# Performance work log

Measured on AMD Instinct MI355X. Metric: run time of the kernel, lower is better.

The kernel has to match this reference:

```python
import jax, jax.numpy as jnp
import numpy as np

B, S, H = 1, 2048, 3584
NH, NKV, D = 16, 8, 256
GROUPS = NH // NKV
WINDOW = 1024
SOFTCAP = 50.0
SCALING = 256.0 ** -0.5  # query_pre_attn_scalar ** -0.5
MASK_VAL = -1e9


def rotate_half(x):
    x1, x2 = jnp.split(x, 2, axis=-1)
    return jnp.concatenate([-x2, x1], axis=-1)


def setup_inputs() -> dict:
    key = jax.random.key(0)
    ks = jax.random.split(key, 5)
    hidden_states = jax.random.normal(ks[0], (B, S, H), dtype=jnp.float32)
    # real rotary embeddings, HF convention: [B, S, head_dim]
    inv_freq = 1.0 / (10000.0 ** (np.arange(0, D, 2, dtype=np.float32) / D))
    freqs = np.arange(S, dtype=np.float32)[:, None] * inv_freq[None, :]  # [S, D/2]
    emb = np.concatenate([freqs, freqs], axis=-1)  # [S, D]
    cos = jnp.asarray(np.cos(emb))[None]  # [1, S, D]
    sin = jnp.asarray(np.sin(emb))[None]
    sc = 1.0 / np.sqrt(H)
    wq = jax.random.normal(ks[1], (NH * D, H), dtype=jnp.float32) * sc
    wk = jax.random.normal(ks[2], (NKV * D, H), dtype=jnp.float32) * sc
    wv = jax.random.normal(ks[3], (NKV * D, H), dtype=jnp.float32) * sc
    wo = jax.random.normal(ks[4], (H, NH * D), dtype=jnp.float32) * (1.0 / np.sqrt(NH * D))
    return {"hidden_states": hidden_states, "cos": cos, "sin": sin,
            "wq": wq, "wk": wk, "wv": wv, "wo": wo}


def reference(hidden_states, cos, sin, wq, wk, wv, wo):
    # QKV projections -> [B, n_heads, S, D]
    q = jnp.einsum('bsh,oh->bso', hidden_states, wq).reshape(B, S, NH, D).transpose(0, 2, 1, 3)
    k = jnp.einsum('bsh,oh->bso', hidden_states, wk).reshape(B, S, NKV, D).transpose(0, 2, 1, 3)
    v = jnp.einsum('bsh,oh->bso', hidden_states, wv).reshape(B, S, NKV, D).transpose(0, 2, 1, 3)
    # RoPE (cos/sin broadcast over head dim)
    c = cos[:, None, :, :]
    s = sin[:, None, :, :]
    q = q * c + rotate_half(q) * s
    k = k * c + rotate_half(k) * s
    # GQA: repeat KV heads
    k = jnp.repeat(k, GROUPS, axis=1)  # [B, NH, S, D]
    v = jnp.repeat(v, GROUPS, axis=1)
    # scores + logit soft-capping (tanh), then causal + sliding-window mask
    scores = jnp.einsum('bhqd,bhkd->bhqk', q, k) * SCALING
    scores = SOFTCAP * jnp.tanh(scores / SOFTCAP)
    idx = jnp.arange(S)
    allowed = (idx[None, :] <= idx[:, None]) & (idx[:, None] - idx[None, :] < WINDOW)  # [S, S]
    scores = jnp.where(allowed[None, None], scores, MASK_VAL)
    p = jax.nn.softmax(scores, axis=-1)
    out = jnp.einsum('bhqk,bhkd->bhqd', p, v)  # [B, NH, S, D]
    out = out.transpose(0, 2, 1, 3).reshape(B, S, NH * D)
    return jnp.einsum('bso,ho->bsh', out, wo)
```

## Files before the change

kernel.cpp:

```cpp
#include <hip/hip_runtime.h>
#include <stdint.h>

#define S_LEN 2048
#define HDIM  3584
#define NHEAD 16
#define NKVH  8
#define DHEAD 256
#define QD    (NHEAD * DHEAD)
#define KD    (NKVH * DHEAD)
#define QKVD  (QD + 2 * KD)
#define WINDOW 1024
#define MASK_VAL (-1e9f)

typedef __bf16 bf16x8 __attribute__((ext_vector_type(8)));
typedef float  f32x4  __attribute__((ext_vector_type(4)));

__device__ __forceinline__ float bf2f(ushort u) {
    union { uint32_t i; float f; } v; v.i = ((uint32_t)u) << 16; return v.f;
}
__device__ __forceinline__ ushort f2bf(float f) {
    union { float f; uint32_t i; } v; v.f = f;
    uint32_t r = (v.i + 0x7FFF + ((v.i >> 16) & 1)) >> 16;
    return (ushort)r;
}
__device__ __forceinline__ void gll16(const ushort* g, ushort* l) {
    __builtin_amdgcn_global_load_lds(
        (const __attribute__((address_space(1))) void*)g,
        (__attribute__((address_space(3))) void*)l, 16, 0, 0);
}

#define N_H8  (S_LEN * HDIM / 8)
#define N_WQ8 (QD * HDIM / 8)
#define N_WK8 (KD * HDIM / 8)
#define N_WO8 (HDIM * QD / 8)
#define N_CVT (N_H8 + N_WQ8 + 2 * N_WK8 + N_WO8)

__global__ __launch_bounds__(256) void cvt5_kernel(
    const float* __restrict__ hid, const float* __restrict__ wq,
    const float* __restrict__ wk,  const float* __restrict__ wv,
    const float* __restrict__ wo,
    ushort* __restrict__ hb, ushort* __restrict__ wb, ushort* __restrict__ ob)
{
    int j = blockIdx.x * blockDim.x + threadIdx.x;
    const float* s; ushort* d;
    if (j < N_H8)                { s = hid; d = hb; }
    else if ((j -= N_H8) < N_WQ8)  { s = wq; d = wb; }
    else if ((j -= N_WQ8) < N_WK8) { s = wk; d = wb + (size_t)QD * HDIM; }
    else if ((j -= N_WK8) < N_WK8) { s = wv; d = wb + (size_t)(QD + KD) * HDIM; }
    else                         { j -= N_WK8; s = wo; d = ob; }
    float4 a = ((const float4*)s)[(size_t)j * 2];
    float4 b = ((const float4*)s)[(size_t)j * 2 + 1];
    ushort tmp[8];
    tmp[0] = f2bf(a.x); tmp[1] = f2bf(a.y); tmp[2] = f2bf(a.z); tmp[3] = f2bf(a.w);
    tmp[4] = f2bf(b.x); tmp[5] = f2bf(b.y); tmp[6] = f2bf(b.z); tmp[7] = f2bf(b.w);
    ((uint4*)d)[j] = *(uint4*)tmp;
}

__global__ __launch_bounds__(256) void cvt_kernel(const float* __restrict__ src,
                                                  ushort* __restrict__ dst, int n8)
{
    int i = blockIdx.x * blockDim.x + threadIdx.x;
    if (i >= n8) return;
    float4 a = ((const float4*)src)[i * 2];
    float4 b = ((const float4*)src)[i * 2 + 1];
    ushort tmp[8];
    tmp[0] = f2bf(a.x); tmp[1] = f2bf(a.y); tmp[2] = f2bf(a.z); tmp[3] = f2bf(a.w);
    tmp[4] = f2bf(b.x); tmp[5] = f2bf(b.y); tmp[6] = f2bf(b.z); tmp[7] = f2bf(b.w);
    ((uint4*)dst)[i] = *(uint4*)tmp;
}

__device__ __forceinline__ void stage_f32(ushort* __restrict__ dst,
                                          const float* __restrict__ src,
                                          int r0, int K, int kt, int t)
{
#pragma unroll
    for (int i = 0; i < 4; i++) {
        int g = t + i * 256;
        int row = g >> 3, c = g & 7;
        float4 f = *(const float4*)(src + (size_t)(r0 + row) * K + kt + c * 4);
        ushort4 u;
        u.x = f2bf(f.x); u.y = f2bf(f.y); u.z = f2bf(f.z); u.w = f2bf(f.w);
        int cl = (c >> 1) ^ ((row >> 1) & 3);
        *(ushort4*)(dst + row * 32 + cl * 8 + (c & 1) * 4) = u;
    }
}

template <typename TA, typename TC>
__global__ __launch_bounds__(256) void gemm_async(const TA* __restrict__ A,
                                                  const ushort* __restrict__ B,
                                                  TC* __restrict__ C,
                                                  int M, int N, int K)
{
    __shared__ __align__(16) ushort As[128 * 32];
    __shared__ __align__(16) ushort Bs[128 * 32];

    const int t    = threadIdx.x;
    const int lane = t & 63;
    const int w    = t >> 6;
    const int l15  = lane & 15;
    const int quad = lane >> 4;
    const int m0   = blockIdx.y * 128;
    const int n0   = blockIdx.x * 128;
    const int wm   = (w >> 1) * 64;
    const int wn   = (w & 1) * 64;
    const int srow = lane >> 2;
    const int scol = ((lane & 3) ^ ((srow >> 1) & 3)) * 8;
    const int sw   = (l15 >> 1) & 3;

    f32x4 acc[4][4] = {};

    for (int kt = 0; kt < K; kt += 32) {
        __syncthreads();
#pragma unroll
        for (int j = 0; j < 2; j++) {
            const int rb = w * 32 + j * 16;
            if constexpr (sizeof(TA) == 2) {
                gll16((const ushort*)A + (size_t)(m0 + rb + srow) * K + kt + scol,
                      As + rb * 32);
            }
            gll16(B + (size_t)(n0 + rb + srow) * K + kt + scol, Bs + rb * 32);
        }
        if constexpr (sizeof(TA) == 4)
            stage_f32(As, (const float*)A, m0, K, kt, t);
        __syncthreads();

        bf16x8 a[4], b[4];
#pragma unroll
        for (int mi = 0; mi < 4; mi++)
            a[mi] = *(const bf16x8*)(As + (wm + mi * 16 + l15) * 32 + (quad ^ sw) * 8);
#pragma unroll
        for (int ni = 0; ni < 4; ni++)
            b[ni] = *(const bf16x8*)(Bs + (wn + ni * 16 + l15) * 32 + (quad ^ sw) * 8);
#pragma unroll
        for (int mi = 0; mi < 4; mi++)
#pragma unroll
            for (int ni = 0; ni < 4; ni++)
                acc[mi][ni] = __builtin_amdgcn_mfma_f32_16x16x32_bf16(
                    a[mi], b[ni], acc[mi][ni], 0, 0, 0);
    }

#pragma unroll
    for (int mi = 0; mi < 4; mi++)
#pragma unroll
        for (int ni = 0; ni < 4; ni++)
#pragma unroll
            for (int r = 0; r < 4; r++) {
                int row = m0 + wm + mi * 16 + quad * 4 + r;
                int col = n0 + wn + ni * 16 + l15;
                float val = acc[mi][ni][r];
                if constexpr (sizeof(TC) == 4) C[(size_t)row * N + col] = val;
                else                           C[(size_t)row * N + col] = f2bf(val);
            }
}

__global__ __launch_bounds__(256) void gemm_sync(const float* __restrict__ A,
                                                 const float* __restrict__ B,
                                                 ushort* __restrict__ C,
                                                 int M, int N, int K)
{
    __shared__ __align__(16) ushort As[128 * 32];
    __shared__ __align__(16) ushort Bs[128 * 32];
    const int t = threadIdx.x, lane = t & 63, w = t >> 6;
    const int l15 = lane & 15, quad = lane >> 4;
    const int sw = (l15 >> 1) & 3;
    const int m0 = blockIdx.y * 128, n0 = blockIdx.x * 128;
    const int wm = (w >> 1) * 64, wn = (w & 1) * 64;
    f32x4 acc[4][4] = {};
    for (int kt = 0; kt < K; kt += 32) {
        __syncthreads();
        stage_f32(As, A, m0, K, kt, t);
        stage_f32(Bs, B, n0, K, kt, t);
        __syncthreads();
        bf16x8 a[4], b[4];
#pragma unroll
        for (int mi = 0; mi < 4; mi++)
            a[mi] = *(const bf16x8*)(As + (wm + mi * 16 + l15) * 32 + (quad ^ sw) * 8);
#pragma unroll
        for (int ni = 0; ni < 4; ni++)
            b[ni] = *(const bf16x8*)(Bs + (wn + ni * 16 + l15) * 32 + (quad ^ sw) * 8);
#pragma unroll
        for (int mi = 0; mi < 4; mi++)
#pragma unroll
            for (int ni = 0; ni < 4; ni++)
                acc[mi][ni] = __builtin_amdgcn_mfma_f32_16x16x32_bf16(
                    a[mi], b[ni], acc[mi][ni], 0, 0, 0);
    }
#pragma unroll
    for (int mi = 0; mi < 4; mi++)
#pragma unroll
        for (int ni = 0; ni < 4; ni++)
#pragma unroll
            for (int r = 0; r < 4; r++)
                C[(size_t)(m0 + wm + mi * 16 + quad * 4 + r) * N +
                  n0 + wn + ni * 16 + l15] = f2bf(acc[mi][ni][r]);
}

__global__ __launch_bounds__(256) void gemm_sync_hf(const ushort* __restrict__ A,
                                                    const float* __restrict__ B,
                                                    float* __restrict__ C,
                                                    int M, int N, int K)
{
    __shared__ __align__(16) ushort As[128 * 32];
    __shared__ __align__(16) ushort Bs[128 * 32];
    const int t = threadIdx.x, lane = t & 63, w = t >> 6;
    const int l15 = lane & 15, quad = lane >> 4;
    const int sw = (l15 >> 1) & 3;
    const int m0 = blockIdx.y * 128, n0 = blockIdx.x * 128;
    const int wm = (w >> 1) * 64, wn = (w & 1) * 64;
    f32x4 acc[4][4] = {};
    for (int kt = 0; kt < K; kt += 32) {
        __syncthreads();
#pragma unroll
        for (int i = 0; i < 2; i++) {
            int g = t + i * 256;
            int row = g >> 2, c = g & 3;
            int cl = c ^ ((row >> 1) & 3);
            *(uint4*)(As + row * 32 + cl * 8) =
                *(const uint4*)(A + (size_t)(m0 + row) * K + kt + c * 8);
        }
        stage_f32(Bs, B, n0, K, kt, t);
        __syncthreads();
        bf16x8 a[4], b[4];
#pragma unroll
        for (int mi = 0; mi < 4; mi++)
            a[mi] = *(const bf16x8*)(As + (wm + mi * 16 + l15) * 32 + (quad ^ sw) * 8);
#pragma unroll
        for (int ni = 0; ni < 4; ni++)
            b[ni] = *(const bf16x8*)(Bs + (wn + ni * 16 + l15) * 32 + (quad ^ sw) * 8);
#pragma unroll
        for (int mi = 0; mi < 4; mi++)
#pragma unroll
            for (int ni = 0; ni < 4; ni++)
                acc[mi][ni] = __builtin_amdgcn_mfma_f32_16x16x32_bf16(
                    a[mi], b[ni], acc[mi][ni], 0, 0, 0);
    }
#pragma unroll
    for (int mi = 0; mi < 4; mi++)
#pragma unroll
        for (int ni = 0; ni < 4; ni++)
#pragma unroll
            for (int r = 0; r < 4; r++)
                C[(size_t)(m0 + wm + mi * 16 + quad * 4 + r) * N +
                  n0 + wn + ni * 16 + l15] = acc[mi][ni][r];
}

__global__ void rope_kernel(ushort* __restrict__ x, int stride,
                            const float* __restrict__ cosb,
                            const float* __restrict__ sinb, int nh)
{
    int idx  = blockIdx.x * blockDim.x + threadIdx.x;
    int d    = idx & 127;
    int rest = idx >> 7;
    int h    = rest & (nh - 1);
    int s    = rest / nh;
    size_t base = (size_t)s * stride + h * DHEAD;
    float c  = cosb[s * DHEAD + d];
    float sn = sinb[s * DHEAD + d];
    float x1 = bf2f(x[base + d]);
    float x2 = bf2f(x[base + d + 128]);
    x[base + d]       = f2bf(x1 * c - x2 * sn);
    x[base + d + 128] = f2bf(x2 * c + x1 * sn);
}

__global__ __launch_bounds__(256) void vtrans_kernel(const ushort* __restrict__ v,
                                                     int stride,
                                                     ushort* __restrict__ vt)
{
    __shared__ __align__(16) ushort tile[64][72];
    int s0 = blockIdx.x * 64, c0 = blockIdx.y * 64;
    int t  = threadIdx.x;
#pragma unroll
    for (int i = 0; i < 2; i++) {
        int cI = t + i * 256;
        int row = cI >> 3, c8 = cI & 7;
        *(uint4*)&tile[row][c8 * 8] =
            *(const uint4*)(v + (size_t)(s0 + row) * stride + c0 + c8 * 8);
    }
    __syncthreads();
#pragma unroll
    for (int i = 0; i < 2; i++) {
        int cI = t + i * 256;
        int crow = cI >> 3, s8 = cI & 7;
        ushort tmp[8];
#pragma unroll
        for (int j = 0; j < 8; j++) tmp[j] = tile[s8 * 8 + j][crow];
        *(uint4*)(vt + (size_t)(c0 + crow) * S_LEN + s0 + s8 * 8) = *(uint4*)tmp;
    }
}

template <typename TO>
__global__ __launch_bounds__(256) void attn_kernel(const ushort* __restrict__ qr, int qstride,
                                                   const ushort* __restrict__ kr, int kstride,
                                                   const ushort* __restrict__ vt,
                                                   TO* __restrict__ out)
{
    __shared__ __align__(16) ushort Ks[64 * 256];
    __shared__ __align__(16) ushort Vs[256 * 64];
    __shared__ __align__(16) ushort Ps[4][16 * 68];

    const int t    = threadIdx.x;
    const int lane = t & 63;
    const int w    = t >> 6;
    const int l15  = lane & 15;
    const int quad = lane >> 4;
    const int q0B  = blockIdx.x * 64;
    const int q0   = q0B + w * 16;
    const int h    = blockIdx.y;
    const int kvh  = h >> 1;

    bf16x8 aQ[8];
    const ushort* qrow = qr + (size_t)(q0 + l15) * qstride + h * DHEAD;
#pragma unroll
    for (int kk = 0; kk < 8; kk++)
        aQ[kk] = *(const bf16x8*)(qrow + kk * 32 + quad * 8);

    f32x4 oacc[16] = {};
    float m_i[4], l_i[4];
#pragma unroll
    for (int r = 0; r < 4; r++) { m_i[r] = -1e30f; l_i[r] = 0.f; }

    int km = q0B - (WINDOW - 1);
    if (km < 0) km = 0;
    km &= ~63;

    for (int kb = km; kb < q0B + 64; kb += 64) {
        __syncthreads();
#pragma unroll
        for (int i = 0; i < 8; i++) {
            int base = i * 256 + w * 64;
            int idx  = base + lane;
            int row = idx >> 5, c = idx & 31;
            int cs = c ^ (row & 7);
            gll16(kr + (size_t)(kb + row) * kstride + kvh * DHEAD + cs * 8,
                  Ks + base * 8);
        }
#pragma unroll
        for (int i = 0; i < 8; i++) {
            int base = i * 256 + w * 64;
            int idx  = base + lane;
            int row = idx >> 3, c = idx & 7;
            int cs = c ^ (row & 7);
            gll16(vt + (size_t)(kvh * DHEAD + row) * S_LEN + kb + cs * 8,
                  Vs + base * 8);
        }
        __syncthreads();

        f32x4 sc[4] = {};
#pragma unroll
        for (int ni = 0; ni < 4; ni++) {
            int row = ni * 16 + l15;
#pragma unroll
            for (int kk = 0; kk < 8; kk++) {
                int cp = (kk * 4 + quad) ^ (row & 7);
                bf16x8 bk = *(const bf16x8*)(Ks + row * 256 + cp * 8);
                sc[ni] = __builtin_amdgcn_mfma_f32_16x16x32_bf16(aQ[kk], bk, sc[ni], 0, 0, 0);
            }
        }

        const bool interior = (kb + 63 <= q0) && (q0 + 15 - kb < WINDOW);
        float p[4][4];
        float mt[4] = { -1e30f, -1e30f, -1e30f, -1e30f };
        if (interior) {
#pragma unroll
            for (int ni = 0; ni < 4; ni++)
#pragma unroll
                for (int r = 0; r < 4; r++) {
                    float e = __expf(sc[ni][r] * 0.0025f);
                    float x = 50.f * (e - 1.f) * __builtin_amdgcn_rcpf(e + 1.f);
                    p[ni][r] = x;
                    mt[r] = fmaxf(mt[r], x);
                }
        } else {
#pragma unroll
            for (int ni = 0; ni < 4; ni++)
#pragma unroll
                for (int r = 0; r < 4; r++) {
                    int qi = q0 + quad * 4 + r;
                    int ki = kb + ni * 16 + l15;
                    float e = __expf(sc[ni][r] * 0.0025f);
                    float x = 50.f * (e - 1.f) * __builtin_amdgcn_rcpf(e + 1.f);
                    bool ok = (ki <= qi) && (qi - ki < WINDOW);
                    x = ok ? x : MASK_VAL;
                    p[ni][r] = x;
                    mt[r] = fmaxf(mt[r], x);
                }
        }
#pragma unroll
        for (int r = 0; r < 4; r++)
#pragma unroll
            for (int off = 1; off < 16; off <<= 1)
                mt[r] = fmaxf(mt[r], __shfl_xor(mt[r], off));

        float alpha[4], rs[4];
#pragma unroll
        for (int r = 0; r < 4; r++) {
            float mn = fmaxf(m_i[r], mt[r]);
            alpha[r] = __expf(m_i[r] - mn);
            m_i[r] = mn;
            rs[r] = 0.f;
        }
#pragma unroll
        for (int ni = 0; ni < 4; ni++)
#pragma unroll
            for (int r = 0; r < 4; r++) {
                float pe = __expf(p[ni][r] - m_i[r]);
                rs[r] += pe;
                Ps[w][(quad * 4 + r) * 68 + ni * 16 + l15] = f2bf(pe);
            }
#pragma unroll
        for (int r = 0; r < 4; r++) {
#pragma unroll
            for (int off = 1; off < 16; off <<= 1)
                rs[r] += __shfl_xor(rs[r], off);
            l_i[r] = l_i[r] * alpha[r] + rs[r];
        }
#pragma unroll
        for (int nd = 0; nd < 16; nd++)
#pragma unroll
            for (int r = 0; r < 4; r++)
                oacc[nd][r] *= alpha[r];

        __asm__ volatile("s_waitcnt lgkmcnt(0)" ::: "memory");

        bf16x8 aP[2];
#pragma unroll
        for (int kk = 0; kk < 2; kk++)
            aP[kk] = *(const bf16x8*)(&Ps[w][l15 * 68 + kk * 32 + quad * 8]);
#pragma unroll
        for (int nd = 0; nd < 16; nd++) {
            int row = nd * 16 + l15;
#pragma unroll
            for (int kk = 0; kk < 2; kk++) {
                int cp = (kk * 4 + quad) ^ (row & 7);
                bf16x8 bv = *(const bf16x8*)(Vs + row * 64 + cp * 8);
                oacc[nd] = __builtin_amdgcn_mfma_f32_16x16x32_bf16(aP[kk], bv, oacc[nd], 0, 0, 0);
            }
        }
    }

#pragma unroll
    for (int r = 0; r < 4; r++) {
        float invl = __builtin_amdgcn_rcpf(l_i[r]);
#pragma unroll
        for (int nd = 0; nd < 16; nd++) {
            int qi = q0 + quad * 4 + r;
            int d  = nd * 16 + l15;
            float val = oacc[nd][r] * invl;
            if constexpr (sizeof(TO) == 4) out[(size_t)qi * QD + h * DHEAD + d] = val;
            else                           out[(size_t)qi * QD + h * DHEAD + d] = f2bf(val);
        }
    }
}

extern "C" void kernel_launch(void* const* d_in, const int* in_sizes, int n_in,
                              void* d_out, int out_size, void* d_ws, size_t ws_size,
                              hipStream_t stream)
{
    const float* hidden = (const float*)d_in[0];
    const float* cosb   = (const float*)d_in[1];
    const float* sinb   = (const float*)d_in[2];
    const float* wq     = (const float*)d_in[3];
    const float* wk     = (const float*)d_in[4];
    const float* wv     = (const float*)d_in[5];
    const float* wo     = (const float*)d_in[6];
    float* outp = (float*)d_out;

    const size_t nH   = (size_t)S_LEN * HDIM;
    const size_t nWQ  = (size_t)QD * HDIM;
    const size_t nWK  = (size_t)KD * HDIM;
    const size_t nWB  = (size_t)QKVD * HDIM;
    const size_t nWO  = (size_t)HDIM * QD;
    const size_t nQKV = (size_t)S_LEN * QKVD;
    const size_t nAT  = (size_t)S_LEN * QD;
    const size_t nVT  = (size_t)S_LEN * KD;

    dim3 blk(256);
    const size_t needA = (nWB + nQKV + nH + nWO) * 2;
    const size_t needB = (nWB + nQKV) * 2;

    if (ws_size >= needA) {
        ushort* wb  = (ushort*)d_ws;
        ushort* qkv = wb + nWB;
        ushort* hb  = qkv + nQKV;
        ushort* ob  = hb + nH;
        ushort* at  = wb;
        ushort* vtb = wb + nAT;

        cvt5_kernel<<<(N_CVT + 255) / 256, blk, 0, stream>>>(hidden, wq, wk, wv, wo, hb, wb, ob);
        gemm_async<ushort, ushort><<<dim3(QKVD / 128, S_LEN / 128), blk, 0, stream>>>(
            hb, wb, qkv, S_LEN, QKVD, HDIM);
        rope_kernel<<<(S_LEN * NHEAD * 128) / 256, blk, 0, stream>>>(qkv, QKVD, cosb, sinb, NHEAD);
        rope_kernel<<<(S_LEN * NKVH * 128) / 256, blk, 0, stream>>>(qkv + QD, QKVD, cosb, sinb, NKVH);
        vtrans_kernel<<<dim3(S_LEN / 64, KD / 64), blk, 0, stream>>>(qkv + QD + KD, QKVD, vtb);
        attn_kernel<ushort><<<dim3(S_LEN / 64, NHEAD), blk, 0, stream>>>(
            qkv, QKVD, qkv + QD, QKVD, vtb, at);
        gemm_async<ushort, float><<<dim3(HDIM / 128, S_LEN / 128), blk, 0, stream>>>(
            at, ob, outp, S_LEN, HDIM, QD);
    } else if (ws_size >= needB) {
        ushort* wb  = (ushort*)d_ws;
        ushort* qkv = wb + nWB;
        ushort* at  = wb;
        ushort* vtb = wb + nAT;
        ushort* ob  = wb + nAT + nVT;

        cvt_kernel<<<(int)(nWQ / 8 / 256), blk, 0, stream>>>(wq, wb, (int)(nWQ / 8));
        cvt_kernel<<<(int)(nWK / 8 / 256), blk, 0, stream>>>(wk, wb + nWQ, (int)(nWK / 8));
        cvt_kernel<<<(int)(nWK / 8 / 256), blk, 0, stream>>>(wv, wb + nWQ + nWK, (int)(nWK / 8));
        gemm_async<float, ushort><<<dim3(QKVD / 128, S_LEN / 128), blk, 0, stream>>>(
            hidden, wb, qkv, S_LEN, QKVD, HDIM);
        cvt_kernel<<<(int)(nWO / 8 / 256), blk, 0, stream>>>(wo, ob, (int)(nWO / 8));
        rope_kernel<<<(S_LEN * NHEAD * 128) / 256, blk, 0, stream>>>(qkv, QKVD, cosb, sinb, NHEAD);
        rope_kernel<<<(S_LEN * NKVH * 128) / 256, blk, 0, stream>>>(qkv + QD, QKVD, cosb, sinb, NKVH);
        vtrans_kernel<<<dim3(S_LEN / 64, KD / 64), blk, 0, stream>>>(qkv + QD + KD, QKVD, vtb);
        attn_kernel<ushort><<<dim3(S_LEN / 64, NHEAD), blk, 0, stream>>>(
            qkv, QKVD, qkv + QD, QKVD, vtb, at);
        gemm_async<ushort, float><<<dim3(HDIM / 128, S_LEN / 128), blk, 0, stream>>>(
            at, ob, outp, S_LEN, HDIM, QD);
    } else {
        ushort* q   = (ushort*)d_ws;
        ushort* k   = q + nAT;
        ushort* v   = k + nVT;
        ushort* vtb = v + nVT;
        ushort* at  = vtb + nVT;

        gemm_sync<<<dim3(QD / 128, S_LEN / 128), blk, 0, stream>>>(hidden, wq, q, S_LEN, QD, HDIM);
        gemm_sync<<<dim3(KD / 128, S_LEN / 128), blk, 0, stream>>>(hidden, wk, k, S_LEN, KD, HDIM);
        gemm_sync<<<dim3(KD / 128, S_LEN / 128), blk, 0, stream>>>(hidden, wv, v, S_LEN, KD, HDIM);
        rope_kernel<<<(S_LEN * NHEAD * 128) / 256, blk, 0, stream>>>(q, QD, cosb, sinb, NHEAD);
        rope_kernel<<<(S_LEN * NKVH * 128) / 256, blk, 0, stream>>>(k, KD, cosb, sinb, NKVH);
        vtrans_kernel<<<dim3(S_LEN / 64, KD / 64), blk, 0, stream>>>(v, KD, vtb);
        attn_kernel<ushort><<<dim3(S_LEN / 64, NHEAD), blk, 0, stream>>>(q, QD, k, KD, vtb, at);
        gemm_sync_hf<<<dim3(HDIM / 128, S_LEN / 128), blk, 0, stream>>>(at, wo, outp, S_LEN, HDIM, QD);
    }
}
```

Baseline: 631.1 us.

## Add 256x256-tile eight-wave GEMM with double-buffered ping-pong phases

Adds a new bf16 MFMA GEMM kernel using 256x256 output tiles, 512 threads and 64-wide K tiles. It double-buffers global-to-LDS async loads across eight sub-phases per K step, with explicit vmcnt waits, barriers and s_setprio around the MFMA bursts. The QKV projection and output projection use it in place of the 128x128 kernel. Larger tiles raise data reuse per LDS load and the phase schedule overlaps loads with compute. The cost is fewer blocks (e.g. 14x8 for the output GEMM), which may leave CUs idle, and a fragile hand-written wait schedule.

```diff
diff --git a/kernel.cpp b/kernel.cpp
--- a/kernel.cpp
+++ b/kernel.cpp
@@ -85,6 +85,133 @@
     }
 }
 
+#define VM6   asm volatile("s_waitcnt vmcnt(6)" ::: "memory")
+#define VM0   asm volatile("s_waitcnt vmcnt(0)" ::: "memory")
+#define LGKM0 asm volatile("s_waitcnt lgkmcnt(0)" ::: "memory")
+#define MFEN  asm volatile("" ::: "memory")
+
+#define PHASE(BUF, QM, QN, LA, LB, STAGE, TWAIT) do {                          \
+    if (LA) {                                                                  \
+      _Pragma("unroll") for (int i_ = 0; i_ < 4; i_++) {                       \
+        int R_ = wm + (QM) * 64 + i_ * 16 + l15;                               \
+        afr[i_][0] = *(const bf16x8*)(&As[BUF][R_ * 64 + ((quad ^ (R_ & 7)) * 8)]);       \
+        afr[i_][1] = *(const bf16x8*)(&As[BUF][R_ * 64 + (((4 + quad) ^ (R_ & 7)) * 8)]); \
+      }                                                                        \
+    }                                                                          \
+    if (LB) {                                                                  \
+      _Pragma("unroll") for (int n_ = 0; n_ < 2; n_++) {                       \
+        int R_ = wn + (QN) * 32 + n_ * 16 + l15;                               \
+        bfr[n_][0] = *(const bf16x8*)(&Bs[BUF][R_ * 64 + ((quad ^ (R_ & 7)) * 8)]);       \
+        bfr[n_][1] = *(const bf16x8*)(&Bs[BUF][R_ * 64 + (((4 + quad) ^ (R_ & 7)) * 8)]); \
+      }                                                                        \
+    }                                                                          \
+    STAGE;                                                                     \
+    MFEN;                                                                      \
+    __builtin_amdgcn_s_barrier();                                              \
+    LGKM0;                                                                     \
+    __builtin_amdgcn_s_setprio(1);                                             \
+    _Pragma("unroll") for (int i_ = 0; i_ < 4; i_++)                           \
+      _Pragma("unroll") for (int n_ = 0; n_ < 2; n_++) {                       \
+        acc[(QM) * 4 + i_][(QN) * 2 + n_] = __builtin_amdgcn_mfma_f32_16x16x32_bf16(  \
+            afr[i_][0], bfr[n_][0], acc[(QM) * 4 + i_][(QN) * 2 + n_], 0, 0, 0);      \
+        acc[(QM) * 4 + i_][(QN) * 2 + n_] = __builtin_amdgcn_mfma_f32_16x16x32_bf16(  \
+            afr[i_][1], bfr[n_][1], acc[(QM) * 4 + i_][(QN) * 2 + n_], 0, 0, 0);      \
+      }                                                                        \
+    __builtin_amdgcn_s_setprio(0);                                             \
+    TWAIT;                                                                     \
+    __builtin_amdgcn_s_barrier();                                              \
+    MFEN;                                                                      \
+  } while (0)
+
+template <typename TC>
+__global__ __launch_bounds__(512, 2) void gemm256(const ushort* __restrict__ A,
+                                                  const ushort* __restrict__ B,
+                                                  TC* __restrict__ C,
+                                                  int M, int N, int K)
+{
+    __shared__ __align__(16) ushort As[2][256 * 64];
+    __shared__ __align__(16) ushort Bs[2][256 * 64];
+
+    const int t    = threadIdx.x;
+    const int lane = t & 63;
+    const int w    = t >> 6;
+    const int l15  = lane & 15;
+    const int quad = lane >> 4;
+    const int m0   = blockIdx.y * 256;
+    const int n0   = blockIdx.x * 256;
+    const int wm   = (w >> 2) * 128;
+    const int wn   = (w & 3) * 64;
+    const int lr8  = lane >> 3;
+    const int sc   = lane & 7;
+
+    f32x4 acc[8][4] = {};
+    bf16x8 afr[4][2], bfr[2][2];
+
+    auto stageA = [&](int buf, int qm, int tile) {
+#pragma unroll
+        for (int i = 0; i < 2; i++) {
+            int cb  = (i * 8 + w) * 8;
+            int lr  = cb + lr8;
+            int row = qm * 64 + (lr & 63) + ((lr >> 6) << 7);
+            int rb  = qm * 64 + (cb & 63) + ((cb >> 6) << 7);
+            gll16(A + (size_t)(m0 + row) * K + tile * 64 + ((sc ^ lr8) * 8),
+                  &As[buf][rb * 64]);
+        }
+    };
+    auto stageB = [&](int buf, int qn, int tile) {
+#pragma unroll
+        for (int i = 0; i < 2; i++) {
+            int cb  = (i * 8 + w) * 8;
+            int lr  = cb + lr8;
+            int row = ((lr >> 5) << 6) + qn * 32 + (lr & 31);
+            int rb  = ((cb >> 5) << 6) + qn * 32 + (cb & 31);
+            gll16(B + (size_t)(n0 + row) * K + tile * 64 + ((sc ^ lr8) * 8),
+                  &Bs[buf][rb * 64]);
+        }
+    };
+
+    stageB(0, 0, 0);
+    stageA(0, 1, 0);
+    stageA(0, 0, 0);
+    stageB(0, 1, 0);
+    stageB(1, 0, 1);
+    stageA(1, 1, 1);
+    VM6;
+    __builtin_amdgcn_s_barrier();
+    MFEN;
+
+    const int NJ = K >> 7;
+    for (int j = 0; j < NJ; ++j) {
+        const int T = 2 * j;
+        const bool tl = (j == NJ - 1);
+        PHASE(0, 0, 0, 1, 1, stageA(1, 0, T + 1), MFEN);
+        PHASE(0, 1, 0, 1, 0, stageB(1, 1, T + 1), if (tl) { VM0; } else { VM6; });
+        PHASE(0, 1, 1, 0, 1, if (!tl) { stageB(0, 0, T + 2); }, MFEN);
+        PHASE(0, 0, 1, 1, 0, if (!tl) { stageA(0, 1, T + 2); }, if (!tl) { VM6; } else { MFEN; });
+        PHASE(1, 0, 0, 1, 1, if (!tl) { stageA(0, 0, T + 2); }, MFEN);
+        PHASE(1, 1, 0, 1, 0, if (!tl) { stageB(0, 1, T + 2); }, if (!tl) { VM6; } else { MFEN; });
+        PHASE(1, 1, 1, 0, 1, if (!tl) { stageB(1, 0, T + 3); }, MFEN);
+        PHASE(1, 0, 1, 1, 0, if (!tl) { stageA(1, 1, T + 3); }, if (!tl) { VM6; } else { MFEN; });
+    }
+
+#pragma unroll
+    for (int qm = 0; qm < 2; qm++)
+#pragma unroll
+      for (int i = 0; i < 4; i++)
+#pragma unroll
+        for (int qn = 0; qn < 2; qn++)
+#pragma unroll
+          for (int n = 0; n < 2; n++)
+#pragma unroll
+            for (int r = 0; r < 4; r++) {
+                int row = m0 + wm + qm * 64 + i * 16 + quad * 4 + r;
+                int col = n0 + wn + qn * 32 + n * 16 + l15;
+                float val = acc[qm * 4 + i][qn * 2 + n][r];
+                if constexpr (sizeof(TC) == 4) C[(size_t)row * N + col] = val;
+                else                           C[(size_t)row * N + col] = f2bf(val);
+            }
+}
+
 template <typename TA, typename TC>
 __global__ __launch_bounds__(256) void gemm_async(const TA* __restrict__ A,
                                                   const ushort* __restrict__ B,
@@ -475,6 +602,7 @@
     const size_t nVT  = (size_t)S_LEN * KD;
 
     dim3 blk(256);
+    dim3 blk512(512);
     const size_t needA = (nWB + nQKV + nH + nWO) * 2;
     const size_t needB = (nWB + nQKV) * 2;
 
@@ -487,14 +615,14 @@
         ushort* vtb = wb + nAT;
 
         cvt5_kernel<<<(N_CVT + 255) / 256, blk, 0, stream>>>(hidden, wq, wk, wv, wo, hb, wb, ob);
-        gemm_async<ushort, ushort><<<dim3(QKVD / 128, S_LEN / 128), blk, 0, stream>>>(
+        gemm256<ushort><<<dim3(QKVD / 256, S_LEN / 256), blk512, 0, stream>>>(
             hb, wb, qkv, S_LEN, QKVD, HDIM);
         rope_kernel<<<(S_LEN * NHEAD * 128) / 256, blk, 0, stream>>>(qkv, QKVD, cosb, sinb, NHEAD);
         rope_kernel<<<(S_LEN * NKVH * 128) / 256, blk, 0, stream>>>(qkv + QD, QKVD, cosb, sinb, NKVH);
         vtrans_kernel<<<dim3(S_LEN / 64, KD / 64), blk, 0, stream>>>(qkv + QD + KD, QKVD, vtb);
         attn_kernel<ushort><<<dim3(S_LEN / 64, NHEAD), blk, 0, stream>>>(
             qkv, QKVD, qkv + QD, QKVD, vtb, at);
-        gemm_async<ushort, float><<<dim3(HDIM / 128, S_LEN / 128), blk, 0, stream>>>(
+        gemm256<float><<<dim3(HDIM / 256, S_LEN / 256), blk512, 0, stream>>>(
             at, ob, outp, S_LEN, HDIM, QD);
     } else if (ws_size >= needB) {
         ushort* wb  = (ushort*)d_ws;
@@ -514,7 +642,7 @@
         vtrans_kernel<<<dim3(S_LEN / 64, KD / 64), blk, 0, stream>>>(qkv + QD + KD, QKVD, vtb);
         attn_kernel<ushort><<<dim3(S_LEN / 64, NHEAD), blk, 0, stream>>>(
             qkv, QKVD, qkv + QD, QKVD, vtb, at);
-        gemm_async<ushort, float><<<dim3(HDIM / 128, S_LEN / 128), blk, 0, stream>>>(
+        gemm256<float><<<dim3(HDIM / 256, S_LEN / 256), blk512, 0, stream>>>(
             at, ob, outp, S_LEN, HDIM, QD);
     } else {
         ushort* q   = (ushort*)d_ws;
```

Result: faster. 562.8 us (-10.8%).

## Add 256-wide double-buffered bf16 GEMM kernel for QKV and output projections

Applied to the files above, without the earlier changes.

Introduces a new 512-thread GEMM with 256xBM tiles, K-step of 64, double-buffered LDS filled by async global-to-LDS loads, split into quadrants so loads for the next tile overlap MFMA work, with an XOR swizzle and s_setprio around the MFMA bursts. It replaces the 128x128 gemm_async for the QKV projection and the output projection. Larger tiles raise arithmetic intensity and cut global traffic, at the cost of more registers and LDS, fewer blocks (the QKV grid is 32x8) and possible wave-quantization issues. The epilogue writes scalar per-element stores.

```diff
diff --git a/kernel.cpp b/kernel.cpp
--- a/kernel.cpp
+++ b/kernel.cpp
@@ -85,6 +85,140 @@
     }
 }
 
+#define VM4   asm volatile("s_waitcnt vmcnt(4)" ::: "memory")
+#define VM3   asm volatile("s_waitcnt vmcnt(3)" ::: "memory")
+#define VM0   asm volatile("s_waitcnt vmcnt(0)" ::: "memory")
+#define MFEN  asm volatile("" ::: "memory")
+
+#define MMAQ(AF, BF, QM, QN) do {                                              \
+    __builtin_amdgcn_s_setprio(1);                                             \
+    _Pragma("unroll") for (int i_ = 0; i_ < MIQ; i_++)                         \
+      _Pragma("unroll") for (int n_ = 0; n_ < 2; n_++) {                       \
+        acc[(QM) * MIQ + i_][(QN) * 2 + n_] = __builtin_amdgcn_mfma_f32_16x16x32_bf16( \
+            AF[i_][0], BF[n_][0], acc[(QM) * MIQ + i_][(QN) * 2 + n_], 0, 0, 0);       \
+        acc[(QM) * MIQ + i_][(QN) * 2 + n_] = __builtin_amdgcn_mfma_f32_16x16x32_bf16( \
+            AF[i_][1], BF[n_][1], acc[(QM) * MIQ + i_][(QN) * 2 + n_], 0, 0, 0);       \
+      }                                                                        \
+    __builtin_amdgcn_s_setprio(0);                                             \
+  } while (0)
+
+template <int BM, typename TC>
+__global__ __launch_bounds__(512, 2) void gemm256(const ushort* __restrict__ A,
+                                                  const ushort* __restrict__ B,
+                                                  TC* __restrict__ C,
+                                                  int M, int N, int K)
+{
+    constexpr int WM  = BM / 2;
+    constexpr int MIQ = WM / 32;
+    __shared__ __align__(16) ushort As[2][BM * 64];
+    __shared__ __align__(16) ushort Bs[2][256 * 64];
+
+    const int t    = threadIdx.x;
+    const int lane = t & 63;
+    const int w    = t >> 6;
+    const int l15  = lane & 15;
+    const int quad = lane >> 4;
+    const int m0   = blockIdx.y * BM;
+    const int n0   = blockIdx.x * 256;
+    const int wm   = (w >> 2) * WM;
+    const int wn   = (w & 3) * 64;
+    const int lr8  = lane >> 3;
+    const int sc   = lane & 7;
+
+    f32x4 acc[2 * MIQ][4] = {};
+    bf16x8 a0f[MIQ][2], a1f[MIQ][2], b0f[2][2], b1f[2][2];
+
+    auto readA = [&](bf16x8 (&af)[MIQ][2], int buf, int qm) {
+#pragma unroll
+        for (int i = 0; i < MIQ; i++) {
+            int R = wm + qm * (WM / 2) + i * 16 + l15;
+            af[i][0] = *(const bf16x8*)(&As[buf][R * 64 + ((quad ^ (R & 7)) * 8)]);
+            af[i][1] = *(const bf16x8*)(&As[buf][R * 64 + (((4 + quad) ^ (R & 7)) * 8)]);
+        }
+    };
+    auto readB = [&](bf16x8 (&bf)[2][2], int buf, int qn) {
+#pragma unroll
+        for (int n = 0; n < 2; n++) {
+            int R = wn + qn * 32 + n * 16 + l15;
+            bf[n][0] = *(const bf16x8*)(&Bs[buf][R * 64 + ((quad ^ (R & 7)) * 8)]);
+            bf[n][1] = *(const bf16x8*)(&Bs[buf][R * 64 + (((4 + quad) ^ (R & 7)) * 8)]);
+        }
+    };
+
+    auto stageA = [&](int buf, int qm, int tile) {
+#pragma unroll
+        for (int i = 0; i < BM / 128; i++) {
+            int cb = (i * 8 + w) * 8;
+            int lr = cb + lr8;
+            int row, rb;
+            if constexpr (BM == 256) {
+                row = qm * 64 + (lr & 63) + ((lr >> 6) << 7);
+                rb  = qm * 64 + (cb & 63) + ((cb >> 6) << 7);
+            } else {
+                row = qm * 32 + (lr & 31) + ((lr >> 5) << 6);
+                rb  = qm * 32 + (cb & 31) + ((cb >> 5) << 6);
+            }
+            gll16(A + (size_t)(m0 + row) * K + tile * 64 + ((sc ^ lr8) * 8),
+                  &As[buf][rb * 64]);
+        }
+    };
+    auto stageB = [&](int buf, int qn, int tile) {
+#pragma unroll
+        for (int i = 0; i < 2; i++) {
+            int cb  = (i * 8 + w) * 8;
+            int lr  = cb + lr8;
+            int row = ((lr >> 5) << 6) + qn * 32 + (lr & 31);
+            int rb  = ((cb >> 5) << 6) + qn * 32 + (cb & 31);
+            gll16(B + (size_t)(n0 + row) * K + tile * 64 + ((sc ^ lr8) * 8),
+                  &Bs[buf][rb * 64]);
+        }
+    };
+
+    const int NT = K >> 6;
+
+    stageA(0, 0, 0); stageB(0, 0, 0); stageB(0, 1, 0); stageA(0, 1, 0);
+    if constexpr (BM == 256) { VM4; } else { VM3; }
+    __builtin_amdgcn_s_barrier(); MFEN;
+
+    for (int T = 0; T < NT; ++T) {
+        const int buf = T & 1;
+        const bool pf = (T + 1 < NT);
+        readB(b0f, buf, 0);
+        readA(a0f, buf, 0);
+        if (pf) { stageA(buf ^ 1, 0, T + 1); stageB(buf ^ 1, 0, T + 1); }
+        MMAQ(a0f, b0f, 0, 0);
+        if (pf) { if constexpr (BM == 256) { VM4; } else { VM3; } } else { VM0; }
+        __builtin_amdgcn_s_barrier(); MFEN;
+        readB(b1f, buf, 1);
+        if (pf) { stageB(buf ^ 1, 1, T + 1); stageA(buf ^ 1, 1, T + 1); }
+        MMAQ(a0f, b1f, 0, 1);
+        readA(a1f, buf, 1);
+        MMAQ(a1f, b1f, 1, 1);
+        MMAQ(a1f, b0f, 1, 0);
+        if (pf) {
+            if constexpr (BM == 256) { VM4; } else { VM3; }
+            __builtin_amdgcn_s_barrier(); MFEN;
+        }
+    }
+
+#pragma unroll
+    for (int qm = 0; qm < 2; qm++)
+#pragma unroll
+      for (int i = 0; i < MIQ; i++)
+#pragma unroll
+        for (int qn = 0; qn < 2; qn++)
+#pragma unroll
+          for (int n = 0; n < 2; n++)
+#pragma unroll
+            for (int r = 0; r < 4; r++) {
+                int row = m0 + wm + qm * (WM / 2) + i * 16 + quad * 4 + r;
+                int col = n0 + wn + qn * 32 + n * 16 + l15;
+                float val = acc[qm * MIQ + i][qn * 2 + n][r];
+                if constexpr (sizeof(TC) == 4) C[(size_t)row * N + col] = val;
+                else                           C[(size_t)row * N + col] = f2bf(val);
+            }
+}
+
 template <typename TA, typename TC>
 __global__ __launch_bounds__(256) void gemm_async(const TA* __restrict__ A,
                                                   const ushort* __restrict__ B,
@@ -475,6 +609,7 @@
     const size_t nVT  = (size_t)S_LEN * KD;
 
     dim3 blk(256);
+    dim3 blk512(512);
     const size_t needA = (nWB + nQKV + nH + nWO) * 2;
     const size_t needB = (nWB + nQKV) * 2;
 
@@ -487,14 +622,14 @@
         ushort* vtb = wb + nAT;
 
         cvt5_kernel<<<(N_CVT + 255) / 256, blk, 0, stream>>>(hidden, wq, wk, wv, wo, hb, wb, ob);
-        gemm_async<ushort, ushort><<<dim3(QKVD / 128, S_LEN / 128), blk, 0, stream>>>(
+        gemm256<256, ushort><<<dim3(QKVD / 256, S_LEN / 256), blk512, 0, stream>>>(
             hb, wb, qkv, S_LEN, QKVD, HDIM);
         rope_kernel<<<(S_LEN * NHEAD * 128) / 256, blk, 0, stream>>>(qkv, QKVD, cosb, sinb, NHEAD);
         rope_kernel<<<(S_LEN * NKVH * 128) / 256, blk, 0, stream>>>(qkv + QD, QKVD, cosb, sinb, NKVH);
         vtrans_kernel<<<dim3(S_LEN / 64, KD / 64), blk, 0, stream>>>(qkv + QD + KD, QKVD, vtb);
         attn_kernel<ushort><<<dim3(S_LEN / 64, NHEAD), blk, 0, stream>>>(
             qkv, QKVD, qkv + QD, QKVD, vtb, at);
-        gemm_async<ushort, float><<<dim3(HDIM / 128, S_LEN / 128), blk, 0, stream>>>(
+        gemm256<128, float><<<dim3(HDIM / 256, S_LEN / 128), blk512, 0, stream>>>(
             at, ob, outp, S_LEN, HDIM, QD);
     } else if (ws_size >= needB) {
         ushort* wb  = (ushort*)d_ws;
@@ -514,7 +649,7 @@
         vtrans_kernel<<<dim3(S_LEN / 64, KD / 64), blk, 0, stream>>>(qkv + QD + KD, QKVD, vtb);
         attn_kernel<ushort><<<dim3(S_LEN / 64, NHEAD), blk, 0, stream>>>(
             qkv, QKVD, qkv + QD, QKVD, vtb, at);
-        gemm_async<ushort, float><<<dim3(HDIM / 128, S_LEN / 128), blk, 0, stream>>>(
+        gemm256<128, float><<<dim3(HDIM / 256, S_LEN / 128), blk512, 0, stream>>>(
             at, ob, outp, S_LEN, HDIM, QD);
     } else {
         ushort* q   = (ushort*)d_ws;
```

New measurement: 547.0 us. 13.3% less time.
